# Optimization experiments

Measured on AMD Instinct MI355X. Metric: run time of the kernel, lower is better.

## Reference

```python
import jax, jax.numpy as jnp
import numpy as np

N, E = 50000, 800000
IN_DIM, HID, OUT = 128, 128, 2


def _sage_conv(x, src, dst, W_l, W_r, b, num_nodes):
    # PyG SAGEConv (mean aggr): out_i = mean_{j in N(i)} x_j @ W_l + x_i @ W_r + b
    msg_sum = jax.ops.segment_sum(x[src], dst, num_segments=num_nodes)  # [N, d]
    deg = jax.ops.segment_sum(jnp.ones((src.shape[0],), x.dtype), dst, num_segments=num_nodes)
    mean = msg_sum / jnp.maximum(deg, 1.0)[:, None]
    return mean @ W_l + x @ W_r + b


def setup_inputs() -> dict:
    key = jax.random.key(0)
    ks = jax.random.split(key, 9)
    s = lambda fin: 1.0 / np.sqrt(fin)
    x = jax.random.normal(ks[0], (N, IN_DIM), jnp.float32)
    edge_index = jax.random.randint(ks[1], (2, E), 0, N, dtype=jnp.int64)
    W1_l = jax.random.uniform(ks[2], (IN_DIM, HID), jnp.float32, -s(IN_DIM), s(IN_DIM))
    W1_r = jax.random.uniform(ks[3], (IN_DIM, HID), jnp.float32, -s(IN_DIM), s(IN_DIM))
    b1 = jnp.zeros((HID,), jnp.float32)
    W2_l = jax.random.uniform(ks[4], (HID, HID), jnp.float32, -s(HID), s(HID))
    W2_r = jax.random.uniform(ks[5], (HID, HID), jnp.float32, -s(HID), s(HID))
    b2 = jnp.zeros((HID,), jnp.float32)
    W_head = jax.random.uniform(ks[6], (HID, OUT), jnp.float32, -s(HID), s(HID))
    b_head = jax.random.uniform(ks[7], (OUT,), jnp.float32, -s(HID), s(HID))
    return {"x": x, "edge_index": edge_index, "W1_l": W1_l, "W1_r": W1_r, "b1": b1,
            "W2_l": W2_l, "W2_r": W2_r, "b2": b2, "W_head": W_head, "b_head": b_head}


def reference(x, edge_index, W1_l, W1_r, b1, W2_l, W2_r, b2, W_head, b_head):
    num_nodes = x.shape[0]
    src, dst = edge_index[0], edge_index[1]
    h = jax.nn.relu(_sage_conv(x, src, dst, W1_l, W1_r, b1, num_nodes))
    h = jax.nn.relu(_sage_conv(h, src, dst, W2_l, W2_r, b2, num_nodes))
    # dropout is identity in eval mode
    return h @ W_head + b_head
```

## Files before the change

### kernel.cpp

```cpp
#include <hip/hip_runtime.h>
#include <hip/hip_bf16.h>

#define DIM 128
#define CAP 64

typedef short short8_t __attribute__((ext_vector_type(8)));
typedef float float4_t __attribute__((ext_vector_type(4)));
typedef float f32x4 __attribute__((ext_vector_type(4)));
typedef unsigned int u32x2 __attribute__((ext_vector_type(2)));

__device__ __forceinline__ unsigned short f2bf(float f) {
    __hip_bfloat16 h = __float2bfloat16(f);
    return *reinterpret_cast<unsigned short*>(&h);
}
__device__ __forceinline__ float bf2f(unsigned int lo16) {
    return __uint_as_float(lo16 << 16);
}

__global__ __launch_bounds__(256) void zero_deg(int* __restrict__ deg, int nz4)
{
    int i = blockIdx.x * 256 + threadIdx.x;
    if (i < nz4) reinterpret_cast<int4*>(deg)[i] = make_int4(0, 0, 0, 0);
}

__global__ __launch_bounds__(256) void fused_build(
    const int* __restrict__ src, const int* __restrict__ dst,
    int* __restrict__ deg, unsigned short* __restrict__ padded,
    const float* __restrict__ x, unsigned short* __restrict__ xB,
    const float* __restrict__ W1l, const float* __restrict__ W1r,
    const float* __restrict__ W2l, const float* __restrict__ W2r,
    unsigned short* __restrict__ Wt1, unsigned short* __restrict__ Wt2,
    int E, int nx4, int ngrp, int eblk)
{
    const int b = blockIdx.x;
    const int EBLKS = eblk * 8;
    if (b < EBLKS) {
        const int g = b & 7;
        const int c = b >> 3;
        const int e = c * 256 + threadIdx.x;
        if (e < E) {
            const int d = __builtin_nontemporal_load(dst + e);
            const int lo = g * ngrp;
            if (d >= lo && d < lo + ngrp) {
                const int s = __builtin_nontemporal_load(src + e);
                int pos = atomicAdd(&deg[d], 1);
                if (pos < CAP) padded[(size_t)d * CAP + pos] = (unsigned short)s;
            }
        }
        return;
    }
    int idx = (b - EBLKS) * 256 + threadIdx.x;
    if (idx < nx4) {
        f32x4 v = __builtin_nontemporal_load(reinterpret_cast<const f32x4*>(x) + idx);
        u32x2 p;
        p.x = (unsigned int)f2bf(v.x) | ((unsigned int)f2bf(v.y) << 16);
        p.y = (unsigned int)f2bf(v.z) | ((unsigned int)f2bf(v.w) << 16);
        __builtin_nontemporal_store(p, reinterpret_cast<u32x2*>(xB) + idx);
        return;
    }
    idx -= nx4;
    if (idx < 65536) {
        const int which = idx >> 15;
        const int j = idx & 32767;
        const int c = j >> 8;
        const int k = j & 255;
        const float* Wl = which ? W2l : W1l;
        const float* Wr = which ? W2r : W1r;
        unsigned short* Wt = which ? Wt2 : Wt1;
        float v = (k < DIM) ? Wl[k * DIM + c] : Wr[(k - DIM) * DIM + c];
        Wt[c * 256 + (k ^ ((c & 7) << 3))] = f2bf(v);
    }
}

__global__ __launch_bounds__(256) void gather_mean_bf(
    const unsigned short* __restrict__ xb, const int* __restrict__ deg,
    const unsigned short* __restrict__ padded, unsigned short* __restrict__ mean, int n)
{
    const int node = (blockIdx.x * 256 + threadIdx.x) >> 6;
    const int lane = threadIdx.x & 63;
    if (node >= n) return;
    int len = deg[node];
    if (len > CAP) len = CAP;
    const unsigned short* row = padded + (size_t)node * CAP;
    const int idxreg = (int)row[lane];
    const int row4 = lane >> 4;
    const int col  = lane & 15;
    const uint4* xv = (const uint4*)xb;
    float a0 = 0.f, a1 = 0.f, a2 = 0.f, a3 = 0.f;
    float a4 = 0.f, a5 = 0.f, a6 = 0.f, a7 = 0.f;

#define LOADQ(EOFF)                                                          \
    {                                                                        \
        const int e = (EOFF) + row4;                                         \
        const bool act = e < len;                                            \
        int si = __shfl(idxreg, e, 64);                                      \
        si = act ? si : 0;                                                   \
        uint4 v = xv[(size_t)si * 16 + col];                                 \
        if (!act) { v.x = 0u; v.y = 0u; v.z = 0u; v.w = 0u; }                \
        a0 += bf2f(v.x & 0xffffu); a1 += bf2f(v.x >> 16);                    \
        a2 += bf2f(v.y & 0xffffu); a3 += bf2f(v.y >> 16);                    \
        a4 += bf2f(v.z & 0xffffu); a5 += bf2f(v.z >> 16);                    \
        a6 += bf2f(v.w & 0xffffu); a7 += bf2f(v.w >> 16);                    \
    }

    LOADQ(0) LOADQ(4) LOADQ(8) LOADQ(12)
    if (len > 16) { LOADQ(16) LOADQ(20) LOADQ(24) LOADQ(28) }
    if (len > 32) { LOADQ(32) LOADQ(36) LOADQ(40) LOADQ(44) }
    if (len > 48) { LOADQ(48) LOADQ(52) LOADQ(56) LOADQ(60) }
#undef LOADQ

    a0 += __shfl_xor(a0, 16, 64); a0 += __shfl_xor(a0, 32, 64);
    a1 += __shfl_xor(a1, 16, 64); a1 += __shfl_xor(a1, 32, 64);
    a2 += __shfl_xor(a2, 16, 64); a2 += __shfl_xor(a2, 32, 64);
    a3 += __shfl_xor(a3, 16, 64); a3 += __shfl_xor(a3, 32, 64);
    a4 += __shfl_xor(a4, 16, 64); a4 += __shfl_xor(a4, 32, 64);
    a5 += __shfl_xor(a5, 16, 64); a5 += __shfl_xor(a5, 32, 64);
    a6 += __shfl_xor(a6, 16, 64); a6 += __shfl_xor(a6, 32, 64);
    a7 += __shfl_xor(a7, 16, 64); a7 += __shfl_xor(a7, 32, 64);
    if (row4 == 0) {
        const float r = 1.0f / fmaxf((float)len, 1.0f);
        uint4 o;
        o.x = (unsigned int)f2bf(a0 * r) | ((unsigned int)f2bf(a1 * r) << 16);
        o.y = (unsigned int)f2bf(a2 * r) | ((unsigned int)f2bf(a3 * r) << 16);
        o.z = (unsigned int)f2bf(a4 * r) | ((unsigned int)f2bf(a5 * r) << 16);
        o.w = (unsigned int)f2bf(a6 * r) | ((unsigned int)f2bf(a7 * r) << 16);
        ((uint4*)mean)[(size_t)node * 16 + col] = o;
    }
}

template <bool FUSE_HEAD>
__global__ __launch_bounds__(256, 2) void sage_dense_mfma(
    const unsigned short* __restrict__ meanB, const unsigned short* __restrict__ xinB,
    const unsigned short* __restrict__ WtS,
    const float* __restrict__ bias,
    unsigned short* __restrict__ outB,
    const float* __restrict__ Wh, const float* __restrict__ bh,
    float* __restrict__ outH,
    int n)
{
    __shared__ unsigned short B_s[32768];
    const int t = threadIdx.x;
    const int node0 = blockIdx.x * 64;
    const int wave = t >> 6;
    const int lane = t & 63;
    const int r = lane & 15;
    const int u = lane >> 4;

    int arow = node0 + wave * 16 + r;
    if (arow >= n) arow = n - 1;
    const unsigned short* aM = meanB + (size_t)arow * DIM + u * 8;
    const unsigned short* aX = xinB + (size_t)arow * DIM + u * 8;

    short8_t a[8];
#pragma unroll
    for (int kk = 0; kk < 4; ++kk) {
        a[kk]     = *reinterpret_cast<const short8_t*>(aM + kk * 32);
        a[kk + 4] = *reinterpret_cast<const short8_t*>(aX + kk * 32);
    }

    {
        const uint4* srcp = reinterpret_cast<const uint4*>(WtS);
        uint4* dstp = reinterpret_cast<uint4*>(B_s);
#pragma unroll
        for (int i = 0; i < 16; ++i) dstp[t + i * 256] = srcp[t + i * 256];
    }
    __syncthreads();

    float4_t acc[8];
#pragma unroll
    for (int ft = 0; ft < 8; ++ft) acc[ft] = (float4_t){0.f, 0.f, 0.f, 0.f};

    const int swz = (r & 7) << 3;
#pragma unroll
    for (int kk = 0; kk < 8; ++kk) {
        const int kbase = (kk * 32 + u * 8) ^ swz;
#pragma unroll
        for (int ft = 0; ft < 8; ++ft) {
            const short8_t b = *reinterpret_cast<const short8_t*>(
                &B_s[(ft * 16 + r) * 256 + kbase]);
            acc[ft] = __builtin_amdgcn_mfma_f32_16x16x32_bf16(a[kk], b, acc[ft], 0, 0, 0);
        }
    }

    if (!FUSE_HEAD) {
#pragma unroll
        for (int ft = 0; ft < 8; ++ft) {
            const int feat = ft * 16 + r;
            const float bv = bias[feat];
#pragma unroll
            for (int j = 0; j < 4; ++j) {
                const int node = node0 + wave * 16 + u * 4 + j;
                if (node < n) {
                    outB[(size_t)node * DIM + feat] = f2bf(fmaxf(acc[ft][j] + bv, 0.0f));
                }
            }
        }
    } else {
        float p0[4] = {0.f, 0.f, 0.f, 0.f};
        float p1[4] = {0.f, 0.f, 0.f, 0.f};
#pragma unroll
        for (int ft = 0; ft < 8; ++ft) {
            const int feat = ft * 16 + r;
            const float bv = bias[feat];
            const float w0 = Wh[feat * 2 + 0];
            const float w1 = Wh[feat * 2 + 1];
#pragma unroll
            for (int j = 0; j < 4; ++j) {
                const float h = fmaxf(acc[ft][j] + bv, 0.0f);
                p0[j] += h * w0;
                p1[j] += h * w1;
            }
        }
#pragma unroll
        for (int off = 1; off < 16; off <<= 1) {
#pragma unroll
            for (int j = 0; j < 4; ++j) {
                p0[j] += __shfl_xor(p0[j], off, 64);
                p1[j] += __shfl_xor(p1[j], off, 64);
            }
        }
        if (r == 0) {
            const float bh0 = bh[0], bh1 = bh[1];
#pragma unroll
            for (int j = 0; j < 4; ++j) {
                const int node = node0 + wave * 16 + u * 4 + j;
                if (node < n) {
                    outH[(size_t)node * 2 + 0] = p0[j] + bh0;
                    outH[(size_t)node * 2 + 1] = p1[j] + bh1;
                }
            }
        }
    }
}

extern "C" void kernel_launch(void* const* d_in, const int* in_sizes, int n_in,
                              void* d_out, int out_size, void* d_ws, size_t ws_size,
                              hipStream_t stream) {
    const float* x    = (const float*)d_in[0];
    const int*   ei   = (const int*)d_in[1];
    const float* W1l  = (const float*)d_in[2];
    const float* W1r  = (const float*)d_in[3];
    const float* b1   = (const float*)d_in[4];
    const float* W2l  = (const float*)d_in[5];
    const float* W2r  = (const float*)d_in[6];
    const float* b2   = (const float*)d_in[7];
    const float* Wh   = (const float*)d_in[8];
    const float* bh   = (const float*)d_in[9];
    float* out = (float*)d_out;

    const int n = in_sizes[0] / DIM;
    const int E = in_sizes[1] / 2;
    const int* src = ei;
    const int* dst = ei + E;

    auto align512 = [](size_t v) { return (v + 511) & ~(size_t)511; };
    char* ws = (char*)d_ws;
    size_t off = 0;
    int* deg      = (int*)(ws + off); off = align512(off + (size_t)n * 4);
    unsigned short* padded = (unsigned short*)(ws + off); off = align512(off + (size_t)n * CAP * 2);
    unsigned short* Wt1 = (unsigned short*)(ws + off); off = align512(off + (size_t)32768 * 2);
    unsigned short* Wt2 = (unsigned short*)(ws + off); off = align512(off + (size_t)32768 * 2);
    unsigned short* xB   = (unsigned short*)(ws + off); off = align512(off + (size_t)n * DIM * 2);
    unsigned short* bufA = (unsigned short*)(ws + off); off = align512(off + (size_t)n * DIM * 2);
    unsigned short* bufB = (unsigned short*)(ws + off); off = align512(off + (size_t)n * DIM * 2);

    const int ggrid = (n + 3) / 4;
    const int mgrid = (n + 63) / 64;

    const int nx4 = n * DIM / 4;
    const int nz4 = n / 4;
    const int zgrid = (nz4 + 255) / 256;
    const int ngrp = (n + 7) / 8;
    const int eblk = (E + 255) / 256;
    const int cgrid = (nx4 + 65536 + 255) / 256;
    const int bgrid = eblk * 8 + cgrid;

    zero_deg<<<zgrid, 256, 0, stream>>>(deg, nz4);
    fused_build<<<bgrid, 256, 0, stream>>>(src, dst, deg, padded, x, xB,
                                           W1l, W1r, W2l, W2r, Wt1, Wt2,
                                           E, nx4, ngrp, eblk);

    gather_mean_bf<<<ggrid, 256, 0, stream>>>(xB, deg, padded, bufA, n);
    sage_dense_mfma<false><<<mgrid, 256, 0, stream>>>(bufA, xB, Wt1, b1, bufB,
                                                      nullptr, nullptr, nullptr, n);

    gather_mean_bf<<<ggrid, 256, 0, stream>>>(bufB, deg, padded, bufA, n);
    sage_dense_mfma<true><<<mgrid, 256, 0, stream>>>(bufA, bufB, Wt2, b2, nullptr,
                                                     Wh, bh, out, n);
}
```

Measured before the change: 136.2 us.

## Build padded adjacency via two-level bucket sort instead of global atomics

Replaces the global-atomic scatter that built per-node padded neighbor lists (with 8x redundant passes over edges) with a counting sort: per-block LDS histograms over 256-node buckets, a prefix scan, a scatter into bucket-sorted order, and a per-bucket pass that fills padded rows using shared-memory atomics. This is meant to eliminate contended global atomics and the repeated edge reads. In exchange it adds three extra kernel launches, a single-block scan, and an intermediate sorted edge buffer. Neighbor order within a row may differ, which changes summation order.

```diff
diff --git a/kernel.cpp b/kernel.cpp
--- a/kernel.cpp
+++ b/kernel.cpp
@@ -3,6 +3,8 @@
 
 #define DIM 128
 #define CAP 64
+#define NB  128
+#define NBK 196
 
 typedef short short8_t __attribute__((ext_vector_type(8)));
 typedef float float4_t __attribute__((ext_vector_type(4)));
@@ -17,39 +19,31 @@
     return __uint_as_float(lo16 << 16);
 }
 
-__global__ __launch_bounds__(256) void zero_deg(int* __restrict__ deg, int nz4)
-{
-    int i = blockIdx.x * 256 + threadIdx.x;
-    if (i < nz4) reinterpret_cast<int4*>(deg)[i] = make_int4(0, 0, 0, 0);
-}
-
-__global__ __launch_bounds__(256) void fused_build(
-    const int* __restrict__ src, const int* __restrict__ dst,
-    int* __restrict__ deg, unsigned short* __restrict__ padded,
+__global__ __launch_bounds__(1024) void build_hist(
+    const int* __restrict__ dst, int* __restrict__ counts,
     const float* __restrict__ x, unsigned short* __restrict__ xB,
     const float* __restrict__ W1l, const float* __restrict__ W1r,
     const float* __restrict__ W2l, const float* __restrict__ W2r,
     unsigned short* __restrict__ Wt1, unsigned short* __restrict__ Wt2,
-    int E, int nx4, int ngrp, int eblk)
-{
+    int E, int epb, int nx4)
+{
+    __shared__ int hist[NBK];
     const int b = blockIdx.x;
-    const int EBLKS = eblk * 8;
-    if (b < EBLKS) {
-        const int g = b & 7;
-        const int c = b >> 3;
-        const int e = c * 256 + threadIdx.x;
-        if (e < E) {
-            const int d = __builtin_nontemporal_load(dst + e);
-            const int lo = g * ngrp;
-            if (d >= lo && d < lo + ngrp) {
-                const int s = __builtin_nontemporal_load(src + e);
-                int pos = atomicAdd(&deg[d], 1);
-                if (pos < CAP) padded[(size_t)d * CAP + pos] = (unsigned short)s;
-            }
-        }
+    const int t = threadIdx.x;
+    if (b < NB) {
+        for (int j = t; j < NBK; j += 1024) hist[j] = 0;
+        __syncthreads();
+        const int beg = b * epb;
+        const int end = min(beg + epb, E);
+        for (int e = beg + t; e < end; e += 1024) {
+            int d = __builtin_nontemporal_load(dst + e);
+            atomicAdd(&hist[d >> 8], 1);
+        }
+        __syncthreads();
+        for (int j = t; j < NBK; j += 1024) counts[j * NB + b] = hist[j];
         return;
     }
-    int idx = (b - EBLKS) * 256 + threadIdx.x;
+    int idx = (b - NB) * 1024 + t;
     if (idx < nx4) {
         f32x4 v = __builtin_nontemporal_load(reinterpret_cast<const f32x4*>(x) + idx);
         u32x2 p;
@@ -69,6 +63,80 @@
         unsigned short* Wt = which ? Wt2 : Wt1;
         float v = (k < DIM) ? Wl[k * DIM + c] : Wr[(k - DIM) * DIM + c];
         Wt[c * 256 + (k ^ ((c & 7) << 3))] = f2bf(v);
+    }
+}
+
+__global__ __launch_bounds__(1024) void scan_counts(
+    int* __restrict__ counts, int* __restrict__ base, int E)
+{
+    __shared__ int s[256];
+    const int t = threadIdx.x;
+    int total = 0;
+    if (t < NBK) {
+        int run = 0;
+        for (int i = 0; i < NB; i += 4) {
+            int4 c = *reinterpret_cast<int4*>(&counts[t * NB + i]);
+            counts[t * NB + i + 0] = run; run += c.x;
+            counts[t * NB + i + 1] = run; run += c.y;
+            counts[t * NB + i + 2] = run; run += c.z;
+            counts[t * NB + i + 3] = run; run += c.w;
+        }
+        total = run;
+    }
+    if (t < 256) s[t] = (t < NBK) ? total : 0;
+    __syncthreads();
+    for (int off = 1; off < 256; off <<= 1) {
+        int v = 0;
+        if (t < 256 && t >= off) v = s[t - off];
+        __syncthreads();
+        if (t < 256) s[t] += v;
+        __syncthreads();
+    }
+    if (t < NBK) base[t] = s[t] - total;
+    if (t == 0) base[NBK] = E;
+}
+
+__global__ __launch_bounds__(1024) void scatter_sorted(
+    const int* __restrict__ src, const int* __restrict__ dst,
+    const int* __restrict__ counts, const int* __restrict__ base,
+    unsigned int* __restrict__ sorted, int E, int epb)
+{
+    __shared__ int cur[NBK];
+    const int b = blockIdx.x;
+    const int t = threadIdx.x;
+    for (int j = t; j < NBK; j += 1024) cur[j] = base[j] + counts[j * NB + b];
+    __syncthreads();
+    const int beg = b * epb;
+    const int end = min(beg + epb, E);
+    for (int e = beg + t; e < end; e += 1024) {
+        int d = __builtin_nontemporal_load(dst + e);
+        int s = __builtin_nontemporal_load(src + e);
+        int pos = atomicAdd(&cur[d >> 8], 1);
+        sorted[pos] = ((unsigned int)(d & 255) << 16) | (unsigned int)s;
+    }
+}
+
+__global__ __launch_bounds__(1024) void build_padded(
+    const unsigned int* __restrict__ sorted, const int* __restrict__ base,
+    unsigned short* __restrict__ padded, int* __restrict__ deg, int n)
+{
+    __shared__ int cur[256];
+    const int b = blockIdx.x;
+    const int t = threadIdx.x;
+    if (t < 256) cur[t] = 0;
+    __syncthreads();
+    const int beg = base[b], end = base[b + 1];
+    for (int e = beg + t; e < end; e += 1024) {
+        unsigned int v = sorted[e];
+        int low = (int)(v >> 16);
+        int rank = atomicAdd(&cur[low], 1);
+        if (rank < CAP)
+            padded[(size_t)(b * 256 + low) * CAP + rank] = (unsigned short)(v & 0xffffu);
+    }
+    __syncthreads();
+    if (t < 256) {
+        int node = b * 256 + t;
+        if (node < n) deg[node] = cur[t];
     }
 }
 
@@ -257,6 +325,9 @@
     char* ws = (char*)d_ws;
     size_t off = 0;
     int* deg      = (int*)(ws + off); off = align512(off + (size_t)n * 4);
+    int* counts   = (int*)(ws + off); off = align512(off + (size_t)NBK * NB * 4);
+    int* base     = (int*)(ws + off); off = align512(off + (size_t)(NBK + 1) * 4);
+    unsigned int* sorted = (unsigned int*)(ws + off); off = align512(off + (size_t)E * 4);
     unsigned short* padded = (unsigned short*)(ws + off); off = align512(off + (size_t)n * CAP * 2);
     unsigned short* Wt1 = (unsigned short*)(ws + off); off = align512(off + (size_t)32768 * 2);
     unsigned short* Wt2 = (unsigned short*)(ws + off); off = align512(off + (size_t)32768 * 2);
@@ -268,17 +339,14 @@
     const int mgrid = (n + 63) / 64;
 
     const int nx4 = n * DIM / 4;
-    const int nz4 = n / 4;
-    const int zgrid = (nz4 + 255) / 256;
-    const int ngrp = (n + 7) / 8;
-    const int eblk = (E + 255) / 256;
-    const int cgrid = (nx4 + 65536 + 255) / 256;
-    const int bgrid = eblk * 8 + cgrid;
-
-    zero_deg<<<zgrid, 256, 0, stream>>>(deg, nz4);
-    fused_build<<<bgrid, 256, 0, stream>>>(src, dst, deg, padded, x, xB,
-                                           W1l, W1r, W2l, W2r, Wt1, Wt2,
-                                           E, nx4, ngrp, eblk);
+    const int epb = (E + NB - 1) / NB;
+    const int hgrid = NB + (nx4 + 65536 + 1023) / 1024;
+
+    build_hist<<<hgrid, 1024, 0, stream>>>(dst, counts, x, xB,
+                                           W1l, W1r, W2l, W2r, Wt1, Wt2, E, epb, nx4);
+    scan_counts<<<1, 1024, 0, stream>>>(counts, base, E);
+    scatter_sorted<<<NB, 1024, 0, stream>>>(src, dst, counts, base, sorted, E, epb);
+    build_padded<<<NBK, 1024, 0, stream>>>(sorted, base, padded, deg, n);
 
     gather_mean_bf<<<ggrid, 256, 0, stream>>>(xB, deg, padded, bufA, n);
     sage_dense_mfma<false><<<mgrid, 256, 0, stream>>>(bufA, xB, Wt1, b1, bufB,
```

Result: faster. 126.5 us (-7.2%).
